# Performance work log

Measured on AMD Instinct MI355X. Metric: run time of the kernel, lower is better.

Reference implementation:

```python
import jax, jax.numpy as jnp
import numpy as np

N, D, K = 32768, 256, 2048
BETA = 0.25  # init arg beta, in [0,1) branch of the loss


def setup_inputs() -> dict:
    key = jax.random.key(0)
    k1, k2 = jax.random.split(key)
    x = jax.random.normal(k1, (N, D), dtype=jnp.float32)
    # mimics nn.Embedding init: uniform(-1/K, 1/K) then mean-centered
    cb = jax.random.uniform(k2, (K, D), dtype=jnp.float32, minval=-1.0 / K, maxval=1.0 / K)
    codebook = cb - cb.mean(axis=0)
    return {"x": x, "codebook": codebook}


def reference(x, codebook):
    # pairwise squared L2 distances: [N, K]
    dist = (
        jnp.sum(x * x, axis=1, keepdims=True)
        + jnp.sum(codebook * codebook, axis=1)
        - 2.0 * jnp.matmul(x, codebook.T)
    )
    encoding_inds = jnp.argmin(dist, axis=1)  # [N]
    # one-hot @ codebook == gather of nearest code vectors
    x_codebook = jnp.take(codebook, encoding_inds, axis=0)  # [N, D]
    # straight-through quantization
    x_quantized = x + jax.lax.stop_gradient(x_codebook - x)
    # VQ loss, beta in [0, 1) branch
    commit = jnp.mean((x - jax.lax.stop_gradient(x_codebook)) ** 2)
    embed = jnp.mean((x_codebook - jax.lax.stop_gradient(x)) ** 2)
    loss = BETA * commit + embed
    return x_quantized, loss
```

## Files before the change

kernel.cpp:

```cpp
#include <hip/hip_runtime.h>

#define N_ROWS 32768
#define DIM    256
#define KCODES 2048
#define CSCALE 4096.0f
#define BROWS  64

typedef __attribute__((ext_vector_type(16))) float f32x16;
typedef __attribute__((ext_vector_type(4)))  unsigned int u32x4;

union frag16 { u32x4 v; long l[2]; };

__device__ __forceinline__ uint4 pack16(const float* s) {
    int a = __builtin_amdgcn_cvt_pk_fp8_f32(s[0],  s[1],  0, false);
    a     = __builtin_amdgcn_cvt_pk_fp8_f32(s[2],  s[3],  a, true);
    int b = __builtin_amdgcn_cvt_pk_fp8_f32(s[4],  s[5],  0, false);
    b     = __builtin_amdgcn_cvt_pk_fp8_f32(s[6],  s[7],  b, true);
    int c = __builtin_amdgcn_cvt_pk_fp8_f32(s[8],  s[9],  0, false);
    c     = __builtin_amdgcn_cvt_pk_fp8_f32(s[10], s[11], c, true);
    int d = __builtin_amdgcn_cvt_pk_fp8_f32(s[12], s[13], 0, false);
    d     = __builtin_amdgcn_cvt_pk_fp8_f32(s[14], s[15], d, true);
    uint4 o; o.x = a; o.y = b; o.z = c; o.w = d;
    return o;
}

__global__ void prep_h(const float* __restrict__ cb,
                       float* __restrict__ halfcn, float* __restrict__ loss) {
    const int t    = threadIdx.x;
    const int code = blockIdx.x * 4 + (t >> 6);
    const int s    = t & 63;
    if (blockIdx.x == 0 && t == 0) *loss = 0.0f;
    const int kc = s >> 4, d = (s >> 2) & 3, b4 = (s & 3) * 4;
    const int h = d >> 1, q = d & 1;
    const int k0 = kc * 64 + q * 32 + (b4 >> 3) * 16 + h * 8 + (b4 & 7);
    float4 v = *(const float4*)&cb[(size_t)code * DIM + k0];
    float ssum = v.x * v.x + v.y * v.y + v.z * v.z + v.w * v.w;
    #pragma unroll
    for (int o = 32; o > 0; o >>= 1) ssum += __shfl_down(ssum, o, 64);
    if (s == 0) halfcn[code] = 0.5f * CSCALE * ssum;
}

__global__ void prep_frag(const float* __restrict__ cb, uint4* __restrict__ cbF) {
    const int gid = blockIdx.x * 256 + threadIdx.x;
    const int L   = gid & 63;
    const int r   = gid >> 6;
    const int j   = r & 1;
    const int ct  = (r >> 1) & 1;
    const int w   = (r >> 2) & 3;
    const int i   = r >> 4;
    const int pass = i >> 2, kc = i & 3;
    const int h   = L >> 5, l32 = L & 31;
    const int code = pass * 256 + w * 64 + ct * 32 + l32;
    float buf[16];
    #pragma unroll
    for (int b = 0; b < 4; b++) {
        const int k0 = kc * 64 + j * 32 + (b >> 1) * 16 + h * 8 + (b & 1) * 4;
        float4 v = *(const float4*)&cb[(size_t)code * DIM + k0];
        buf[b * 4 + 0] = v.x * CSCALE; buf[b * 4 + 1] = v.y * CSCALE;
        buf[b * 4 + 2] = v.z * CSCALE; buf[b * 4 + 3] = v.w * CSCALE;
    }
    cbF[gid] = pack16(buf);
}

__global__ __launch_bounds__(256, 2) void vq_fused(
        const float* __restrict__ x, const float* __restrict__ cb,
        const uint4* __restrict__ cbF, const float* __restrict__ halfcn,
        float* __restrict__ out, float* __restrict__ loss) {
    __shared__ char As[4][4096];
    __shared__ float hcs[KCODES];
    struct Tail { float red[BROWS][4]; int idxs[BROWS]; float lred[4]; };
    Tail* tl = (Tail*)As;

    const int t    = threadIdx.x;
    const int lane = t & 63;
    const int w    = t >> 6;
    const int l32  = lane & 31;
    const int h    = lane >> 5;
    const int row0 = blockIdx.x * BROWS;

    {
        const int r   = t >> 2;
        const int kc  = t & 3;
        const int key = (r >> 1) & 3;
        const float* src = x + (size_t)(row0 + r) * DIM + kc * 64;
        float buf[16];
        #pragma unroll
        for (int p = 0; p < 4; p++) {
            const int d = p ^ key, hh = d >> 1, qq = d & 1;
            #pragma unroll
            for (int j = 0; j < 4; j++) *(float4*)(buf + j * 4) =
                *(const float4*)(src + qq * 32 + (j >> 1) * 16 + hh * 8 + (j & 1) * 4);
            *(uint4*)(As[kc] + r * 64 + p * 16) = pack16(buf);
        }
        #pragma unroll
        for (int jj = 0; jj < 8; jj++) hcs[jj * 256 + t] = halfcn[jj * 256 + t];
    }

    const int key = (l32 >> 1) & 3;
    const int p0  = (h * 2 + 0) ^ key;
    const int p1  = (h * 2 + 1) ^ key;

    float mp[2][16];
    #pragma unroll
    for (int rt = 0; rt < 2; rt++)
        #pragma unroll
        for (int r = 0; r < 16; r++) mp[rt][r] = -3.0e38f;

    const char* bbase = (const char*)cbF + w * 4096 + (size_t)lane * 16;

    frag16 bfr[2][8];
    #pragma unroll
    for (int s = 0; s < 2; s++)
        #pragma unroll
        for (int u = 0; u < 2; u++)
            #pragma unroll
            for (int c = 0; c < 4; c++)
                bfr[s][u * 4 + c].v =
                    *(const u32x4*)(bbase + (s * 2 + u) * 16384 + c * 1024);

    __syncthreads();

    frag16 afr[4][2][2];
    #pragma unroll
    for (int kc = 0; kc < 4; kc++) {
        const char* ab = As[kc];
        #pragma unroll
        for (int rt = 0; rt < 2; rt++) {
            const int rbase = (rt * 32 + l32) * 64;
            afr[kc][rt][0].v = *(const u32x4*)(ab + rbase + p0 * 16);
            afr[kc][rt][1].v = *(const u32x4*)(ab + rbase + p1 * 16);
        }
    }

    #pragma unroll
    for (int pass = 0; pass < 8; ++pass) {
        const float hc0 = hcs[pass * 256 + w * 64 + l32];
        const float hc1 = hcs[pass * 256 + w * 64 + 32 + l32];
        f32x16 acc[2][2];
        #pragma unroll
        for (int rt = 0; rt < 2; rt++)
            #pragma unroll
            for (int r = 0; r < 16; r++) {
                acc[rt][0][r] = -hc0;
                acc[rt][1][r] = -hc1;
            }

        #pragma unroll
        for (int kc2 = 0; kc2 < 2; ++kc2) {
            const int pair = pass * 2 + kc2;
            const int sl   = pair & 1;

            #pragma unroll
            for (int u = 0; u < 2; u++) {
                const int kc = kc2 * 2 + u;
                #pragma unroll
                for (int q = 0; q < 2; q++)
                    #pragma unroll
                    for (int hf = 0; hf < 2; hf++)
                        #pragma unroll
                        for (int rt = 0; rt < 2; rt++)
                            #pragma unroll
                            for (int ct = 0; ct < 2; ct++)
                                acc[rt][ct] = __builtin_amdgcn_mfma_f32_32x32x16_fp8_fp8(
                                    afr[kc][rt][q].l[hf], bfr[sl][u * 4 + ct * 2 + q].l[hf],
                                    acc[rt][ct], 0, 0, 0);
                if (pair + 2 < 16) {
                    #pragma unroll
                    for (int c = 0; c < 4; c++)
                        bfr[sl][u * 4 + c].v = *(const u32x4*)(
                            bbase + ((pair + 2) * 2 + u) * 16384 + c * 1024);
                }
            }
        }

        #pragma unroll
        for (int ct = 0; ct < 2; ct++) {
            const unsigned code = (unsigned)(pass * 256 + w * 64 + ct * 32 + l32);
            #pragma unroll
            for (int rt = 0; rt < 2; rt++)
                #pragma unroll
                for (int r = 0; r < 16; r++) {
                    unsigned u = (__float_as_uint(acc[rt][ct][r]) & 0xFFFFF800u) | code;
                    mp[rt][r] = fmaxf(mp[rt][r], __uint_as_float(u));
                }
        }
    }

    #pragma unroll
    for (int m = 1; m <= 16; m <<= 1)
        #pragma unroll
        for (int rt = 0; rt < 2; rt++)
            #pragma unroll
            for (int r = 0; r < 16; r++)
                mp[rt][r] = fmaxf(mp[rt][r], __shfl_xor(mp[rt][r], m, 64));

    __syncthreads();

    if (l32 == 0) {
        #pragma unroll
        for (int rt = 0; rt < 2; rt++)
            #pragma unroll
            for (int r = 0; r < 16; r++) {
                const int row = rt * 32 + (r & 3) + 8 * (r >> 2) + 4 * h;
                tl->red[row][w] = mp[rt][r];
            }
    }
    __syncthreads();
    if (t < BROWS) {
        float b0 = fmaxf(fmaxf(tl->red[t][0], tl->red[t][1]),
                         fmaxf(tl->red[t][2], tl->red[t][3]));
        tl->idxs[t] = (int)(__float_as_uint(b0) & 2047u);
    }
    __syncthreads();

    float lsum = 0.0f;
    #pragma unroll 4
    for (int r = 0; r < BROWS; r++) {
        const int code = tl->idxs[r];
        const float c  = cb[(size_t)code * DIM + t];
        const float xv = x[(size_t)(row0 + r) * DIM + t];
        out[(size_t)(row0 + r) * DIM + t] = c;
        const float d = xv - c;
        lsum += d * d;
    }
    #pragma unroll
    for (int o = 32; o > 0; o >>= 1) lsum += __shfl_down(lsum, o, 64);
    if (lane == 0) tl->lred[w] = lsum;
    __syncthreads();
    if (t == 0) {
        const float scale = 1.25f / (float)((size_t)N_ROWS * DIM);
        atomicAdd(loss, (tl->lred[0] + tl->lred[1] + tl->lred[2] + tl->lred[3]) * scale);
    }
}

extern "C" void kernel_launch(void* const* d_in, const int* in_sizes, int n_in,
                              void* d_out, int out_size, void* d_ws, size_t ws_size,
                              hipStream_t stream) {
    const float* x  = (const float*)d_in[0];
    const float* cb = (const float*)d_in[1];
    float* out  = (float*)d_out;
    float* loss = out + (size_t)N_ROWS * DIM;

    char* ws = (char*)d_ws;
    uint4* cbF    = (uint4*)ws;
    float* halfcn = (float*)(ws + (size_t)KCODES * 256);

    prep_h   <<<KCODES / 4, 256, 0, stream>>>(cb, halfcn, loss);
    prep_frag<<<128,        256, 0, stream>>>(cb, cbF);
    vq_fused <<<N_ROWS / BROWS, 256, 0, stream>>>(x, cb, cbF, halfcn, out, loss);
}
```

Baseline: 122.5 us.

## Switch distance GEMM to scaled 32x32x64 FP8 MFMA with new fragment layout

Replaces the 32x32x16 FP8 MFMA instruction with the gfx950 scaled 32x32x64 f8f6f4 MFMA, which needs a quarter as many matrix instructions per tile. To feed 32-byte operands, the codebook fragment layout in prep_frag, the XOR-swizzled LDS layout for x, and the per-wave code assignment are all reworked. Each wave now owns a contiguous range of 16 code tiles instead of interleaved passes. The scale arguments are set to unity (127), and correctness depends on the new operand layouts matching what the instruction expects.

```diff
diff --git a/kernel.cpp b/kernel.cpp
--- a/kernel.cpp
+++ b/kernel.cpp
@@ -7,9 +7,10 @@
 #define BROWS  64
 
 typedef __attribute__((ext_vector_type(16))) float f32x16;
+typedef __attribute__((ext_vector_type(8)))  int   i32x8;
 typedef __attribute__((ext_vector_type(4)))  unsigned int u32x4;
 
-union frag16 { u32x4 v; long l[2]; };
+union frag32 { i32x8 v8; u32x4 q[2]; };
 
 __device__ __forceinline__ uint4 pack16(const float* s) {
     int a = __builtin_amdgcn_cvt_pk_fp8_f32(s[0],  s[1],  0, false);
@@ -30,9 +31,7 @@
     const int code = blockIdx.x * 4 + (t >> 6);
     const int s    = t & 63;
     if (blockIdx.x == 0 && t == 0) *loss = 0.0f;
-    const int kc = s >> 4, d = (s >> 2) & 3, b4 = (s & 3) * 4;
-    const int h = d >> 1, q = d & 1;
-    const int k0 = kc * 64 + q * 32 + (b4 >> 3) * 16 + h * 8 + (b4 & 7);
+    const int k0 = s * 4;
     float4 v = *(const float4*)&cb[(size_t)code * DIM + k0];
     float ssum = v.x * v.x + v.y * v.y + v.z * v.z + v.w * v.w;
     #pragma unroll
@@ -41,21 +40,20 @@
 }
 
 __global__ void prep_frag(const float* __restrict__ cb, uint4* __restrict__ cbF) {
-    const int gid = blockIdx.x * 256 + threadIdx.x;
-    const int L   = gid & 63;
-    const int r   = gid >> 6;
-    const int j   = r & 1;
-    const int ct  = (r >> 1) & 1;
-    const int w   = (r >> 2) & 3;
-    const int i   = r >> 4;
-    const int pass = i >> 2, kc = i & 3;
-    const int h   = L >> 5, l32 = L & 31;
-    const int code = pass * 256 + w * 64 + ct * 32 + l32;
+    const int gid  = blockIdx.x * 256 + threadIdx.x;
+    const int tile = gid >> 9;
+    const int r9   = gid & 511;
+    const int c    = r9 >> 7;
+    const int r7   = r9 & 127;
+    const int u    = r7 >> 6;
+    const int L    = r7 & 63;
+    const int l32  = L & 31, h = L >> 5;
+    const int code = tile * 32 + l32;
+    const int k0   = c * 64 + h * 32 + u * 16;
     float buf[16];
     #pragma unroll
     for (int b = 0; b < 4; b++) {
-        const int k0 = kc * 64 + j * 32 + (b >> 1) * 16 + h * 8 + (b & 1) * 4;
-        float4 v = *(const float4*)&cb[(size_t)code * DIM + k0];
+        float4 v = *(const float4*)&cb[(size_t)code * DIM + k0 + b * 4];
         buf[b * 4 + 0] = v.x * CSCALE; buf[b * 4 + 1] = v.y * CSCALE;
         buf[b * 4 + 2] = v.z * CSCALE; buf[b * 4 + 3] = v.w * CSCALE;
     }
@@ -66,7 +64,7 @@
         const float* __restrict__ x, const float* __restrict__ cb,
         const uint4* __restrict__ cbF, const float* __restrict__ halfcn,
         float* __restrict__ out, float* __restrict__ loss) {
-    __shared__ char As[4][4096];
+    __shared__ char As[2][8192];
     __shared__ float hcs[KCODES];
     struct Tail { float red[BROWS][4]; int idxs[BROWS]; float lred[4]; };
     Tail* tl = (Tail*)As;
@@ -77,113 +75,92 @@
     const int l32  = lane & 31;
     const int h    = lane >> 5;
     const int row0 = blockIdx.x * BROWS;
+    char* asb = &As[0][0];
 
     {
-        const int r   = t >> 2;
-        const int kc  = t & 3;
-        const int key = (r >> 1) & 3;
-        const float* src = x + (size_t)(row0 + r) * DIM + kc * 64;
+        const int r  = t >> 2;
+        const int q4 = t & 3;
+        const int rt = r >> 5, rw = r & 31;
+        const float* src = x + (size_t)(row0 + r) * DIM;
         float buf[16];
         #pragma unroll
-        for (int p = 0; p < 4; p++) {
-            const int d = p ^ key, hh = d >> 1, qq = d & 1;
-            #pragma unroll
-            for (int j = 0; j < 4; j++) *(float4*)(buf + j * 4) =
-                *(const float4*)(src + qq * 32 + (j >> 1) * 16 + hh * 8 + (j & 1) * 4);
-            *(uint4*)(As[kc] + r * 64 + p * 16) = pack16(buf);
+        for (int g = 0; g < 4; g++) {
+            const int o16 = q4 * 4 + g;
+            #pragma unroll
+            for (int j = 0; j < 4; j++)
+                *(float4*)(buf + j * 4) = *(const float4*)(src + o16 * 16 + j * 4);
+            *(uint4*)(asb + rt * 8192 + rw * 256 + ((o16 ^ (rw & 7)) << 4)) = pack16(buf);
         }
         #pragma unroll
         for (int jj = 0; jj < 8; jj++) hcs[jj * 256 + t] = halfcn[jj * 256 + t];
     }
 
-    const int key = (l32 >> 1) & 3;
-    const int p0  = (h * 2 + 0) ^ key;
-    const int p1  = (h * 2 + 1) ^ key;
-
     float mp[2][16];
     #pragma unroll
     for (int rt = 0; rt < 2; rt++)
         #pragma unroll
         for (int r = 0; r < 16; r++) mp[rt][r] = -3.0e38f;
 
-    const char* bbase = (const char*)cbF + w * 4096 + (size_t)lane * 16;
-
-    frag16 bfr[2][8];
+    const char* bbase = (const char*)cbF + (size_t)(w * 16) * 8192 + (size_t)lane * 16;
+
+    frag32 bfr[2][4];
     #pragma unroll
     for (int s = 0; s < 2; s++)
         #pragma unroll
-        for (int u = 0; u < 2; u++)
+        for (int c = 0; c < 4; c++)
+            #pragma unroll
+            for (int u = 0; u < 2; u++)
+                bfr[s][c].q[u] = *(const u32x4*)(bbase + s * 8192 + c * 2048 + u * 1024);
+
+    __syncthreads();
+
+    frag32 afr[4][2];
+    #pragma unroll
+    for (int c = 0; c < 4; c++)
+        #pragma unroll
+        for (int rt = 0; rt < 2; rt++)
+            #pragma unroll
+            for (int u = 0; u < 2; u++) {
+                const int o16 = c * 4 + h * 2 + u;
+                afr[c][rt].q[u] = *(const u32x4*)(
+                    asb + rt * 8192 + l32 * 256 + ((o16 ^ (l32 & 7)) << 4));
+            }
+
+    #pragma unroll
+    for (int tt = 0; tt < 16; ++tt) {
+        const int sl = tt & 1;
+        const float hc = hcs[(w * 16 + tt) * 32 + l32];
+        f32x16 acc[2];
+        #pragma unroll
+        for (int r = 0; r < 16; r++) { acc[0][r] = -hc; acc[1][r] = -hc; }
+
+        #pragma unroll
+        for (int c = 0; c < 4; c++)
+            #pragma unroll
+            for (int rt = 0; rt < 2; rt++)
+                acc[rt] = __builtin_amdgcn_mfma_scale_f32_32x32x64_f8f6f4(
+                    afr[c][rt].v8, bfr[sl][c].v8, acc[rt],
+                    0, 0,
+                    0, 127,
+                    0, 127);
+
+        if (tt + 2 < 16) {
             #pragma unroll
             for (int c = 0; c < 4; c++)
-                bfr[s][u * 4 + c].v =
-                    *(const u32x4*)(bbase + (s * 2 + u) * 16384 + c * 1024);
-
-    __syncthreads();
-
-    frag16 afr[4][2][2];
-    #pragma unroll
-    for (int kc = 0; kc < 4; kc++) {
-        const char* ab = As[kc];
-        #pragma unroll
-        for (int rt = 0; rt < 2; rt++) {
-            const int rbase = (rt * 32 + l32) * 64;
-            afr[kc][rt][0].v = *(const u32x4*)(ab + rbase + p0 * 16);
-            afr[kc][rt][1].v = *(const u32x4*)(ab + rbase + p1 * 16);
+                #pragma unroll
+                for (int u = 0; u < 2; u++)
+                    bfr[sl][c].q[u] = *(const u32x4*)(
+                        bbase + (tt + 2) * 8192 + c * 2048 + u * 1024);
         }
-    }
-
-    #pragma unroll
-    for (int pass = 0; pass < 8; ++pass) {
-        const float hc0 = hcs[pass * 256 + w * 64 + l32];
-        const float hc1 = hcs[pass * 256 + w * 64 + 32 + l32];
-        f32x16 acc[2][2];
+
+        const unsigned code = (unsigned)((w * 16 + tt) * 32 + l32);
         #pragma unroll
         for (int rt = 0; rt < 2; rt++)
             #pragma unroll
             for (int r = 0; r < 16; r++) {
-                acc[rt][0][r] = -hc0;
-                acc[rt][1][r] = -hc1;
+                unsigned u = (__float_as_uint(acc[rt][r]) & 0xFFFFF800u) | code;
+                mp[rt][r] = fmaxf(mp[rt][r], __uint_as_float(u));
             }
-
-        #pragma unroll
-        for (int kc2 = 0; kc2 < 2; ++kc2) {
-            const int pair = pass * 2 + kc2;
-            const int sl   = pair & 1;
-
-            #pragma unroll
-            for (int u = 0; u < 2; u++) {
-                const int kc = kc2 * 2 + u;
-                #pragma unroll
-                for (int q = 0; q < 2; q++)
-                    #pragma unroll
-                    for (int hf = 0; hf < 2; hf++)
-                        #pragma unroll
-                        for (int rt = 0; rt < 2; rt++)
-                            #pragma unroll
-                            for (int ct = 0; ct < 2; ct++)
-                                acc[rt][ct] = __builtin_amdgcn_mfma_f32_32x32x16_fp8_fp8(
-                                    afr[kc][rt][q].l[hf], bfr[sl][u * 4 + ct * 2 + q].l[hf],
-                                    acc[rt][ct], 0, 0, 0);
-                if (pair + 2 < 16) {
-                    #pragma unroll
-                    for (int c = 0; c < 4; c++)
-                        bfr[sl][u * 4 + c].v = *(const u32x4*)(
-                            bbase + ((pair + 2) * 2 + u) * 16384 + c * 1024);
-                }
-            }
-        }
-
-        #pragma unroll
-        for (int ct = 0; ct < 2; ct++) {
-            const unsigned code = (unsigned)(pass * 256 + w * 64 + ct * 32 + l32);
-            #pragma unroll
-            for (int rt = 0; rt < 2; rt++)
-                #pragma unroll
-                for (int r = 0; r < 16; r++) {
-                    unsigned u = (__float_as_uint(acc[rt][ct][r]) & 0xFFFFF800u) | code;
-                    mp[rt][r] = fmaxf(mp[rt][r], __uint_as_float(u));
-                }
-        }
     }
 
     #pragma unroll
```

Result: no change. 123.7 us (+1.0%).
